# Kernel tuning notes

Hardware: AMD Instinct MI355X
Metric: run time of the kernel (lower is better)

Reference implementation:

```python
import jax, jax.numpy as jnp
import numpy as np
import math

B, L, OBS, ACT = 2, 1024, 64, 16
OE, AE, RE, TE = 512, 256, 128, 128
C, H, NL, FF = 1024, 16, 4, 4096
DH = C // H


def setup_inputs():
    key = jax.random.key(0)
    ks = jax.random.split(key, 20)
    def nrm(k, shape, std=1.0):
        return jax.random.normal(k, shape, jnp.float32) * std
    kb = jax.random.split(ks[19], 12)
    return {
        'obs_seq': nrm(ks[0], (B, L, OBS)),
        'act_seq': nrm(ks[1], (B, L, ACT)),
        'rew_seq': nrm(ks[2], (B, L, 1)),
        'obs_W': nrm(ks[3], (OBS, OE), OBS ** -0.5), 'obs_b': jnp.zeros((OE,)),
        'act_W': nrm(ks[4], (ACT, AE), ACT ** -0.5), 'act_b': jnp.zeros((AE,)),
        'rew_W': nrm(ks[5], (1, RE), 1.0), 'rew_b': jnp.zeros((RE,)),
        'tr_W': nrm(ks[6], (OBS, TE), OBS ** -0.5), 'tr_b': jnp.zeros((TE,)),
        'bn_gamma': jnp.ones((OBS,)), 'bn_beta': jnp.zeros((OBS,)),
        'ln1_w': jnp.ones((NL, C)), 'ln1_b': jnp.zeros((NL, C)),
        'qkv_W': nrm(kb[0], (NL, C, 3 * C), C ** -0.5), 'qkv_b': jnp.zeros((NL, 3 * C)),
        'out_W': nrm(kb[1], (NL, C, C), C ** -0.5), 'out_b': jnp.zeros((NL, C)),
        'ln2_w': jnp.ones((NL, C)), 'ln2_b': jnp.zeros((NL, C)),
        'fc_W': nrm(kb[2], (NL, C, FF), C ** -0.5), 'fc_b': jnp.zeros((NL, FF)),
        'pj_W': nrm(kb[3], (NL, FF, C), FF ** -0.5), 'pj_b': jnp.zeros((NL, C)),
    }


def _ln(x, w, b):
    m = x.mean(-1, keepdims=True)
    v = ((x - m) ** 2).mean(-1, keepdims=True)
    return (x - m) * jax.lax.rsqrt(v + 1e-5) * w + b


def _forward(obs_seq, act_seq, rew_seq, obs_W, obs_b, act_W, act_b, rew_W, rew_b,
             tr_W, tr_b, bn_gamma, bn_beta, ln1_w, ln1_b, qkv_W, qkv_b, out_W, out_b,
             ln2_w, ln2_b, fc_W, fc_b, pj_W, pj_b):
    # transition branch: prepend first obs, take deltas; BatchNorm1d in training
    # mode uses biased batch stats over (batch, time) per channel.
    full_obs = jnp.concatenate([obs_seq[:, :1], obs_seq], axis=1)  # (B, L+1, OBS)
    obs2 = full_obs[:, :-1]
    tran = full_obs[:, 1:] - full_obs[:, :-1]  # (B, L, OBS)
    tm = tran.mean((0, 1))
    tv = ((tran - tm) ** 2).mean((0, 1))
    tran = (tran - tm) * jax.lax.rsqrt(tv + 1e-5) * bn_gamma + bn_beta
    # encoder_activation is identity
    enc = jnp.concatenate([
        obs2 @ obs_W + obs_b,
        act_seq @ act_W + act_b,
        rew_seq @ rew_W + rew_b,
        tran @ tr_W + tr_b,
    ], axis=-1)  # (B, L, C)
    mask = jnp.tril(jnp.ones((L, L), dtype=bool))

    def block(x, p):
        l1w, l1b, qW, qb, oW, ob, l2w, l2b, fW, fb, pW, pb = p
        h = _ln(x, l1w, l1b)
        q, k, v = jnp.split(h @ qW + qb, 3, axis=-1)
        q, k, v = (t.reshape(B, L, H, DH).transpose(0, 2, 1, 3) for t in (q, k, v))
        s = jnp.einsum('bhqd,bhkd->bhqk', q, k) / math.sqrt(DH)
        s = jnp.where(mask, s, -jnp.inf)
        a = jax.nn.softmax(s, axis=-1)
        o = jnp.einsum('bhqk,bhkd->bhqd', a, v).transpose(0, 2, 1, 3).reshape(B, L, C)
        x = x + o @ oW + ob  # residual + out_proj
        h2 = _ln(x, l2w, l2b)
        x = x + jax.nn.relu(h2 @ fW + fb) @ pW + pb  # MLP residual
        return x, None

    x, _ = jax.lax.scan(block, enc, (ln1_w, ln1_b, qkv_W, qkv_b, out_W, out_b,
                                     ln2_w, ln2_b, fc_W, fc_b, pj_W, pj_b))
    return jnp.tanh(x)


def reference(obs_seq, act_seq, rew_seq, obs_W, obs_b, act_W, act_b, rew_W, rew_b,
              tr_W, tr_b, bn_gamma, bn_beta, ln1_w, ln1_b, qkv_W, qkv_b, out_W, out_b,
              ln2_w, ln2_b, fc_W, fc_b, pj_W, pj_b):
    return _forward(obs_seq, act_seq, rew_seq, obs_W, obs_b, act_W, act_b, rew_W, rew_b,
                    tr_W, tr_b, bn_gamma, bn_beta, ln1_w, ln1_b, qkv_W, qkv_b, out_W, out_b,
                    ln2_w, ln2_b, fc_W, fc_b, pj_W, pj_b)
```

## Files before the change

### kernel.cpp

```cpp
#include <hip/hip_runtime.h>
#include <hip/hip_bf16.h>
#include <math.h>

constexpr int kB   = 2;
constexpr int kL   = 1024;
constexpr int kOBS = 64;
constexpr int kACT = 16;
constexpr int kC   = 1024;
constexpr int kH   = 16;
constexpr int kDH  = 64;
constexpr int kFF  = 4096;
constexpr int kNL  = 4;
constexpr int kRows = kB * kL;
constexpr int kOE = 512, kAE = 256, kRE = 128, kTE = 128;

typedef _Float16 f16x8 __attribute__((ext_vector_type(8)));
typedef _Float16 f16x4 __attribute__((ext_vector_type(4)));
typedef float    f32x4 __attribute__((ext_vector_type(4)));

__device__ __forceinline__ unsigned short f2h(float x) {
    return __builtin_bit_cast(unsigned short, (_Float16)x);
}
__device__ __forceinline__ float h2f(unsigned short x) {
    return (float)__builtin_bit_cast(_Float16, x);
}
__device__ __forceinline__ void gload_lds16(const void* g, void* l) {
    __builtin_amdgcn_global_load_lds(
        (const __attribute__((address_space(1))) unsigned int*)g,
        (__attribute__((address_space(3))) unsigned int*)l, 16, 0, 0);
}

__global__ __launch_bounds__(256) void tran_stats_kernel(
    const float* __restrict__ obs, float* __restrict__ tm, float* __restrict__ tv)
{
    const int f = blockIdx.x;
    const int tid = threadIdx.x;
    float sum = 0.f, sq = 0.f;
    for (int r = tid; r < kRows; r += 256) {
        const int t = r & (kL - 1);
        float d = 0.f;
        if (t > 0) {
            const float cur  = obs[(size_t)r * kOBS + f];
            const float prev = obs[(size_t)(r - 1) * kOBS + f];
            d = cur - prev;
        }
        sum += d; sq += d * d;
    }
    for (int off = 32; off > 0; off >>= 1) {
        sum += __shfl_down(sum, off);
        sq  += __shfl_down(sq, off);
    }
    __shared__ float sa[4], sb[4];
    if ((tid & 63) == 0) { sa[tid >> 6] = sum; sb[tid >> 6] = sq; }
    __syncthreads();
    if (tid == 0) {
        const float ts = sa[0] + sa[1] + sa[2] + sa[3];
        const float tq = sb[0] + sb[1] + sb[2] + sb[3];
        const float m = ts / (float)kRows;
        tm[f] = m;
        tv[f] = tq / (float)kRows - m * m;
    }
}

__global__ __launch_bounds__(256) void encode_kernel(
    const float* __restrict__ obs, const float* __restrict__ act, const float* __restrict__ rew,
    const float* __restrict__ obs_W, const float* __restrict__ obs_b,
    const float* __restrict__ act_W, const float* __restrict__ act_b,
    const float* __restrict__ rew_W, const float* __restrict__ rew_b,
    const float* __restrict__ tr_W,  const float* __restrict__ tr_b,
    const float* __restrict__ bn_g,  const float* __restrict__ bn_b,
    const float* __restrict__ tm,    const float* __restrict__ tv,
    float* __restrict__ enc)
{
    const int row = blockIdx.x;
    const int t = row & (kL - 1);
    const int tid = threadIdx.x;
    __shared__ float s_obs2[kOBS];
    __shared__ float s_tran[kOBS];
    __shared__ float s_act[kACT];
    __shared__ float s_rew;
    if (tid < kOBS) {
        const float cur  = obs[(size_t)row * kOBS + tid];
        const float prev = (t > 0) ? obs[(size_t)(row - 1) * kOBS + tid] : cur;
        s_obs2[tid] = prev;
        const float tr = cur - prev;
        s_tran[tid] = (tr - tm[tid]) * rsqrtf(tv[tid] + 1e-5f) * bn_g[tid] + bn_b[tid];
    } else if (tid < kOBS + kACT) {
        s_act[tid - kOBS] = act[(size_t)row * kACT + (tid - kOBS)];
    } else if (tid == kOBS + kACT) {
        s_rew = rew[row];
    }
    __syncthreads();
    float* er = enc + (size_t)row * kC;
    #pragma unroll
    for (int s = 0; s < 4; ++s) {
        const int c = tid + s * 256;
        float v;
        if (c < kOE) {
            v = obs_b[c];
            #pragma unroll
            for (int k = 0; k < kOBS; ++k) v += s_obs2[k] * obs_W[k * kOE + c];
        } else if (c < kOE + kAE) {
            const int cc = c - kOE;
            v = act_b[cc];
            #pragma unroll
            for (int k = 0; k < kACT; ++k) v += s_act[k] * act_W[k * kAE + cc];
        } else if (c < kOE + kAE + kRE) {
            const int cc = c - (kOE + kAE);
            v = s_rew * rew_W[cc] + rew_b[cc];
        } else {
            const int cc = c - (kOE + kAE + kRE);
            v = tr_b[cc];
            #pragma unroll
            for (int k = 0; k < kOBS; ++k) v += s_tran[k] * tr_W[k * kTE + cc];
        }
        er[c] = v;
    }
}

__global__ __launch_bounds__(256) void ln_kernel(
    const float* __restrict__ x, const float* __restrict__ w,
    const float* __restrict__ b, unsigned short* __restrict__ out)
{
    const int row = blockIdx.x;
    const int tid = threadIdx.x;
    const float4 xv = *reinterpret_cast<const float4*>(&x[(size_t)row * kC + tid * 4]);
    float s = xv.x + xv.y + xv.z + xv.w;
    float q = xv.x * xv.x + xv.y * xv.y + xv.z * xv.z + xv.w * xv.w;
    for (int off = 32; off > 0; off >>= 1) {
        s += __shfl_down(s, off);
        q += __shfl_down(q, off);
    }
    __shared__ float sa[4], sb[4];
    if ((tid & 63) == 0) { sa[tid >> 6] = s; sb[tid >> 6] = q; }
    __syncthreads();
    const float ts = sa[0] + sa[1] + sa[2] + sa[3];
    const float tq = sb[0] + sb[1] + sb[2] + sb[3];
    const float mean = ts * (1.f / kC);
    const float var  = tq * (1.f / kC) - mean * mean;
    const float rstd = rsqrtf(var + 1e-5f);
    const float4 wv = *reinterpret_cast<const float4*>(&w[tid * 4]);
    const float4 bv = *reinterpret_cast<const float4*>(&b[tid * 4]);
    ushort4 o;
    o.x = f2h((xv.x - mean) * rstd * wv.x + bv.x);
    o.y = f2h((xv.y - mean) * rstd * wv.y + bv.y);
    o.z = f2h((xv.z - mean) * rstd * wv.z + bv.z);
    o.w = f2h((xv.w - mean) * rstd * wv.w + bv.w);
    *reinterpret_cast<ushort4*>(&out[(size_t)row * kC + tid * 4]) = o;
}

__global__ __launch_bounds__(256) void reduce_ln_kernel(
    const unsigned short* __restrict__ part,
    const float* __restrict__ w, const float* __restrict__ b,
    float* __restrict__ x, unsigned short* __restrict__ h)
{
    const int row = blockIdx.x;
    const int tid = threadIdx.x;
    const size_t base = (size_t)row * kC + tid * 4;
    float4 xv = *reinterpret_cast<const float4*>(&x[base]);
    #pragma unroll
    for (int z = 0; z < 4; ++z) {
        const ushort4 p = *reinterpret_cast<const ushort4*>(
            &part[(size_t)z * kRows * kC + base]);
        xv.x += h2f(p.x); xv.y += h2f(p.y); xv.z += h2f(p.z); xv.w += h2f(p.w);
    }
    *reinterpret_cast<float4*>(&x[base]) = xv;

    float s = xv.x + xv.y + xv.z + xv.w;
    float q = xv.x * xv.x + xv.y * xv.y + xv.z * xv.z + xv.w * xv.w;
    for (int off = 32; off > 0; off >>= 1) {
        s += __shfl_down(s, off);
        q += __shfl_down(q, off);
    }
    __shared__ float sa[4], sb[4];
    if ((tid & 63) == 0) { sa[tid >> 6] = s; sb[tid >> 6] = q; }
    __syncthreads();
    const float ts = sa[0] + sa[1] + sa[2] + sa[3];
    const float tq = sb[0] + sb[1] + sb[2] + sb[3];
    const float mean = ts * (1.f / kC);
    const float var  = tq * (1.f / kC) - mean * mean;
    const float rstd = rsqrtf(var + 1e-5f);
    const float4 wv = *reinterpret_cast<const float4*>(&w[tid * 4]);
    const float4 bv = *reinterpret_cast<const float4*>(&b[tid * 4]);
    ushort4 o;
    o.x = f2h((xv.x - mean) * rstd * wv.x + bv.x);
    o.y = f2h((xv.y - mean) * rstd * wv.y + bv.y);
    o.z = f2h((xv.z - mean) * rstd * wv.z + bv.z);
    o.w = f2h((xv.w - mean) * rstd * wv.w + bv.w);
    *reinterpret_cast<ushort4*>(&h[base]) = o;
}

__global__ __launch_bounds__(256) void reduce_tanh_kernel(
    const unsigned short* __restrict__ part, float* __restrict__ x)
{
    const size_t base = ((size_t)blockIdx.x * 256 + threadIdx.x) * 4;
    float4 xv = *reinterpret_cast<const float4*>(&x[base]);
    #pragma unroll
    for (int z = 0; z < 4; ++z) {
        const ushort4 p = *reinterpret_cast<const ushort4*>(
            &part[(size_t)z * kRows * kC + base]);
        xv.x += h2f(p.x); xv.y += h2f(p.y); xv.z += h2f(p.z); xv.w += h2f(p.w);
    }
    xv.x = tanhf(xv.x); xv.y = tanhf(xv.y); xv.z = tanhf(xv.z); xv.w = tanhf(xv.w);
    *reinterpret_cast<float4*>(&x[base]) = xv;
}

__device__ __forceinline__ void convT_tile(
    const float* __restrict__ W, unsigned short* __restrict__ WT,
    int K, int N, int k0, int n0, int tid)
{
    __shared__ unsigned short t[64][68];
    const int r = tid >> 4, c4 = (tid & 15) * 4;
    #pragma unroll
    for (int s = 0; s < 4; ++s) {
        const int rr = r + s * 16;
        const float4 v = *reinterpret_cast<const float4*>(&W[(size_t)(k0 + rr) * N + n0 + c4]);
        t[rr][c4 + 0] = f2h(v.x);
        t[rr][c4 + 1] = f2h(v.y);
        t[rr][c4 + 2] = f2h(v.z);
        t[rr][c4 + 3] = f2h(v.w);
    }
    __syncthreads();
    #pragma unroll
    for (int s = 0; s < 4; ++s) {
        const int rn = r + s * 16;
        ushort4 o;
        o.x = t[c4 + 0][rn];
        o.y = t[c4 + 1][rn];
        o.z = t[c4 + 2][rn];
        o.w = t[c4 + 3][rn];
        *reinterpret_cast<ushort4*>(&WT[(size_t)(n0 + rn) * K + k0 + c4]) = o;
    }
}

__global__ __launch_bounds__(256) void convert_layer_kernel(
    const float* __restrict__ qW, const float* __restrict__ oW,
    const float* __restrict__ fW, const float* __restrict__ pW,
    unsigned short* __restrict__ qWT, unsigned short* __restrict__ oWT,
    unsigned short* __restrict__ fWT, unsigned short* __restrict__ pWT)
{
    int bid = blockIdx.x;
    const int tid = threadIdx.x;
    if (bid < 768)  {
        convT_tile(qW, qWT, 1024, 3072, (bid / 48) * 64, (bid % 48) * 64, tid);
    } else if (bid < 1024) {
        bid -= 768;
        convT_tile(oW, oWT, 1024, 1024, (bid / 16) * 64, (bid % 16) * 64, tid);
    } else if (bid < 2048) {
        bid -= 1024;
        convT_tile(fW, fWT, 1024, 4096, (bid / 64) * 64, (bid % 64) * 64, tid);
    } else {
        bid -= 2048;
        convT_tile(pW, pWT, 4096, 1024, (bid / 16) * 64, (bid % 16) * 64, tid);
    }
}

template<int RELU, int RES, int MODE>
__global__ __launch_bounds__(256) void gemm_f16_kernel(
    const unsigned short* __restrict__ A,
    const unsigned short* __restrict__ BT,
    const float* __restrict__ bias,
    float* __restrict__ Cf, unsigned short* __restrict__ Ch,
    unsigned short* __restrict__ Cv,
    int M, int N, int K)
{
    __shared__ __align__(16) unsigned short As[2][128 * 64];
    __shared__ __align__(16) unsigned short Bs[2][128 * 64];
    const int tid = threadIdx.x;
    const int lane = tid & 63;
    const int wv   = tid >> 6;
    const int wr = wv >> 1, wc = wv & 1;

    const int nx  = gridDim.x;
    const int nxy = gridDim.x * gridDim.y;
    int flat = blockIdx.x + nx * blockIdx.y + nxy * blockIdx.z;
    const int cpx = (nxy * gridDim.z) >> 3;
    flat = (flat & 7) * cpx + (flat >> 3);
    const int bx = flat % nx;
    const int by = (flat / nx) % gridDim.y;
    const int bz = flat / nxy;

    const int bm = by * 128;
    const int bn = bx * 128;
    const int ksz  = K / gridDim.z;
    const int kbeg = bz * ksz;
    const int kend = kbeg + ksz;

    const int grow = tid >> 3;
    const int gs   = (tid & 7) ^ (grow & 7);

    const int fr = lane & 15;
    const int kb = lane >> 4;

    auto stage = [&](int k0, int buf) {
        #pragma unroll
        for (int c = 0; c < 4; ++c) {
            gload_lds16(A  + (size_t)(bm + c * 32 + grow) * K + k0 + gs * 8,
                        (char*)&As[buf][0] + c * 4096 + wv * 1024);
            gload_lds16(BT + (size_t)(bn + c * 32 + grow) * K + k0 + gs * 8,
                        (char*)&Bs[buf][0] + c * 4096 + wv * 1024);
        }
    };

    f32x4 acc[4][4] = {};

    stage(kbeg, 0);
    __syncthreads();
    int cur = 0;
    for (int k0 = kbeg; k0 < kend; k0 += 64) {
        f16x8 a[2][4], b[2][4];
        #pragma unroll
        for (int kf = 0; kf < 2; ++kf) {
            #pragma unroll
            for (int m = 0; m < 4; ++m) {
                const int row = wr * 64 + m * 16 + fr;
                a[kf][m] = *reinterpret_cast<const f16x8*>(
                    &As[cur][row * 64 + (((kf * 4 + kb) ^ (row & 7)) * 8)]);
            }
            #pragma unroll
            for (int n = 0; n < 4; ++n) {
                const int row = wc * 64 + n * 16 + fr;
                b[kf][n] = *reinterpret_cast<const f16x8*>(
                    &Bs[cur][row * 64 + (((kf * 4 + kb) ^ (row & 7)) * 8)]);
            }
        }
        if (k0 + 64 < kend) stage(k0 + 64, cur ^ 1);
        #pragma unroll
        for (int kf = 0; kf < 2; ++kf)
            #pragma unroll
            for (int m = 0; m < 4; ++m)
                #pragma unroll
                for (int n = 0; n < 4; ++n)
                    acc[m][n] = __builtin_amdgcn_mfma_f32_16x16x32_f16(
                        a[kf][m], b[kf][n], acc[m][n], 0, 0, 0);

        __syncthreads();
        cur ^= 1;
    }

    const int fq = lane >> 4;
    if (MODE == 5) {
        unsigned short* pp = Ch + (size_t)bz * M * N;
        const bool addb = (bz == 0);
        #pragma unroll
        for (int n = 0; n < 4; ++n) {
            const int c = bn + wc * 64 + n * 16 + fr;
            const float bv = addb ? bias[c] : 0.f;
            #pragma unroll
            for (int m = 0; m < 4; ++m) {
                #pragma unroll
                for (int j = 0; j < 4; ++j) {
                    const int r = bm + wr * 64 + m * 16 + fq * 4 + j;
                    pp[(size_t)r * N + c] = f2h(acc[m][n][j] + bv);
                }
            }
        }
        return;
    }
    if (MODE == 2) {
        if (bn < 2 * kC) {
            #pragma unroll
            for (int n = 0; n < 4; ++n) {
                const int c = bn + wc * 64 + n * 16 + fr;
                const float bv = bias[c];
                #pragma unroll
                for (int m = 0; m < 4; ++m) {
                    #pragma unroll
                    for (int j = 0; j < 4; ++j) {
                        const int r = bm + wr * 64 + m * 16 + fq * 4 + j;
                        Ch[(size_t)r * (2 * kC) + c] = f2h(acc[m][n][j] + bv);
                    }
                }
            }
        } else {
            #pragma unroll
            for (int n = 0; n < 4; ++n) {
                const int c  = bn + wc * 64 + n * 16 + fr;
                const int cc = c - 2 * kC;
                const int hh = cc >> 6, dd = cc & 63;
                const float bv = bias[c];
                #pragma unroll
                for (int m = 0; m < 4; ++m) {
                    const int rr = bm + wr * 64 + m * 16 + fq * 4;
                    const int bb = rr >> 10, t0 = rr & 1023;
                    f16x4 pk;
                    #pragma unroll
                    for (int j = 0; j < 4; ++j) pk[j] = (_Float16)(acc[m][n][j] + bv);
                    *reinterpret_cast<f16x4*>(
                        &Cv[((size_t)(bb * kH + hh) * kDH + dd) * kL + t0]) = pk;
                }
            }
        }
        return;
    }
    #pragma unroll
    for (int n = 0; n < 4; ++n) {
        const int c = bn + wc * 64 + n * 16 + fr;
        const float bv = bias[c];
        #pragma unroll
        for (int m = 0; m < 4; ++m) {
            #pragma unroll
            for (int j = 0; j < 4; ++j) {
                const int r = bm + wr * 64 + m * 16 + fq * 4 + j;
                float v = acc[m][n][j] + bv;
                if (RES)  v += Cf[(size_t)r * N + c];
                if (RELU) v = fmaxf(v, 0.f);
                if (MODE == 1) Ch[(size_t)r * N + c] = f2h(v);
                else           Cf[(size_t)r * N + c] = v;
            }
        }
    }
}

__device__ __forceinline__ int swz(int row, int slot) {
    return row * 64 + ((slot ^ (row & 7)) * 8);
}

__global__ __launch_bounds__(256) void attn_mfma_kernel(
    const unsigned short* __restrict__ qk,
    const unsigned short* __restrict__ vt,
    unsigned short* __restrict__ o)
{
    const int bid = blockIdx.x;
    const int bh  = bid & 31;
    const int qb  = ((bid >> 5) + bh) & 15;
    const int b   = bh >> 4;
    const int h   = bh & 15;
    const int tid  = threadIdx.x;
    const int lane = tid & 63;
    const int wv   = tid >> 6;
    const int fr = lane & 15;
    const int g  = lane >> 4;

    __shared__ __align__(16) unsigned short Ks[64 * 64];
    __shared__ __align__(16) unsigned short Vts[64 * 64];
    __shared__ __align__(16) unsigned short Ps[64 * 64];

    const int qlo = qb * 64;
    const int qg_row = qlo + wv * 16 + fr;

    f16x8 qfrag[2];
    {
        const unsigned short* qg = &qk[(size_t)(b * kL + qg_row) * (2 * kC) + h * kDH];
        #pragma unroll
        for (int kf = 0; kf < 2; ++kf) {
            f16x8 v = *reinterpret_cast<const f16x8*>(&qg[(kf * 4 + g) * 8]);
            #pragma unroll
            for (int i = 0; i < 8; ++i) v[i] *= (_Float16)0.125f;
            qfrag[kf] = v;
        }
    }

    const int sr = tid >> 2;
    const int ss = tid & 3;
    const unsigned short* kbase = &qk[(size_t)(b * kL) * (2 * kC) + kC + h * kDH];
    const unsigned short* vbase = &vt[(size_t)(b * kH + h) * kDH * kL];

    f16x8 kc0 = *reinterpret_cast<const f16x8*>(&kbase[(size_t)sr * (2 * kC) + ss * 8]);
    f16x8 kc1 = *reinterpret_cast<const f16x8*>(&kbase[(size_t)sr * (2 * kC) + (ss + 4) * 8]);
    f16x8 vc0 = *reinterpret_cast<const f16x8*>(&vbase[(size_t)sr * kL + ss * 8]);
    f16x8 vc1 = *reinterpret_cast<const f16x8*>(&vbase[(size_t)sr * kL + (ss + 4) * 8]);

    float m = -INFINITY, l = 0.f;
    f32x4 acc_o[4] = {};

    for (int k0 = 0; k0 <= qlo; k0 += 64) {
        asm volatile("s_waitcnt lgkmcnt(0)" ::: "memory");
        __builtin_amdgcn_sched_barrier(0);
        __builtin_amdgcn_s_barrier();
        __builtin_amdgcn_sched_barrier(0);

        *reinterpret_cast<f16x8*>(&Ks[swz(sr, ss)])      = kc0;
        *reinterpret_cast<f16x8*>(&Ks[swz(sr, ss + 4)])  = kc1;
        *reinterpret_cast<f16x8*>(&Vts[swz(sr, ss)])     = vc0;
        *reinterpret_cast<f16x8*>(&Vts[swz(sr, ss + 4)]) = vc1;

        if (k0 + 64 <= qlo) {
            kc0 = *reinterpret_cast<const f16x8*>(&kbase[(size_t)(k0 + 64 + sr) * (2 * kC) + ss * 8]);
            kc1 = *reinterpret_cast<const f16x8*>(&kbase[(size_t)(k0 + 64 + sr) * (2 * kC) + (ss + 4) * 8]);
            vc0 = *reinterpret_cast<const f16x8*>(&vbase[(size_t)sr * kL + k0 + 64 + ss * 8]);
            vc1 = *reinterpret_cast<const f16x8*>(&vbase[(size_t)sr * kL + k0 + 64 + (ss + 4) * 8]);
        }

        asm volatile("s_waitcnt lgkmcnt(0)" ::: "memory");
        __builtin_amdgcn_sched_barrier(0);
        __builtin_amdgcn_s_barrier();
        __builtin_amdgcn_sched_barrier(0);

        f32x4 acc_s[4] = {};
        #pragma unroll
        for (int kf = 0; kf < 2; ++kf) {
            #pragma unroll
            for (int n = 0; n < 4; ++n) {
                const f16x8 kfr = *reinterpret_cast<const f16x8*>(&Ks[swz(n * 16 + fr, kf * 4 + g)]);
                acc_s[n] = __builtin_amdgcn_mfma_f32_16x16x32_f16(kfr, qfrag[kf], acc_s[n], 0, 0, 0);
            }
        }

        if (k0 == qlo) {
            #pragma unroll
            for (int n = 0; n < 4; ++n)
                #pragma unroll
                for (int j = 0; j < 4; ++j)
                    if (k0 + n * 16 + g * 4 + j > qg_row) acc_s[n][j] = -INFINITY;
        }

        float mx = -INFINITY;
        #pragma unroll
        for (int n = 0; n < 4; ++n)
            #pragma unroll
            for (int j = 0; j < 4; ++j) mx = fmaxf(mx, acc_s[n][j]);
        mx = fmaxf(mx, __shfl_xor(mx, 16));
        mx = fmaxf(mx, __shfl_xor(mx, 32));
        const float mn  = fmaxf(m, mx);
        const float fac = __expf(m - mn);
        float p[4][4];
        float psum = 0.f;
        #pragma unroll
        for (int n = 0; n < 4; ++n)
            #pragma unroll
            for (int j = 0; j < 4; ++j) { p[n][j] = __expf(acc_s[n][j] - mn); psum += p[n][j]; }
        psum += __shfl_xor(psum, 16);
        psum += __shfl_xor(psum, 32);
        l = l * fac + psum;
        m = mn;
        #pragma unroll
        for (int dt = 0; dt < 4; ++dt)
            #pragma unroll
            for (int j = 0; j < 4; ++j) acc_o[dt][j] *= fac;

        #pragma unroll
        for (int n = 0; n < 4; ++n) {
            f16x4 pk;
            #pragma unroll
            for (int j = 0; j < 4; ++j) pk[j] = (_Float16)p[n][j];
            *reinterpret_cast<f16x4*>(&Ps[swz(wv * 16 + fr, 2 * n + (g >> 1)) + (g & 1) * 4]) = pk;
        }

        #pragma unroll
        for (int kf = 0; kf < 2; ++kf) {
            const f16x8 pf = *reinterpret_cast<const f16x8*>(&Ps[swz(wv * 16 + fr, kf * 4 + g)]);
            #pragma unroll
            for (int dt = 0; dt < 4; ++dt) {
                const f16x8 vf = *reinterpret_cast<const f16x8*>(&Vts[swz(dt * 16 + fr, kf * 4 + g)]);
                acc_o[dt] = __builtin_amdgcn_mfma_f32_16x16x32_f16(vf, pf, acc_o[dt], 0, 0, 0);
            }
        }
    }

    const float rl = 1.f / l;
    unsigned short* ob = &o[(size_t)(b * kL + qg_row) * kC + h * kDH];
    #pragma unroll
    for (int dt = 0; dt < 4; ++dt) {
        f16x4 pk;
        #pragma unroll
        for (int j = 0; j < 4; ++j) pk[j] = (_Float16)(acc_o[dt][j] * rl);
        *reinterpret_cast<f16x4*>(&ob[dt * 16 + g * 4]) = pk;
    }
}

extern "C" void kernel_launch(void* const* d_in, const int* in_sizes, int n_in,
                              void* d_out, int out_size, void* d_ws, size_t ws_size,
                              hipStream_t stream)
{
    (void)in_sizes; (void)n_in; (void)out_size; (void)ws_size;
    const float* obs    = (const float*)d_in[0];
    const float* act    = (const float*)d_in[1];
    const float* rew    = (const float*)d_in[2];
    const float* obs_W  = (const float*)d_in[3];
    const float* obs_b  = (const float*)d_in[4];
    const float* act_W  = (const float*)d_in[5];
    const float* act_b  = (const float*)d_in[6];
    const float* rew_W  = (const float*)d_in[7];
    const float* rew_b  = (const float*)d_in[8];
    const float* tr_W   = (const float*)d_in[9];
    const float* tr_b   = (const float*)d_in[10];
    const float* bn_g   = (const float*)d_in[11];
    const float* bn_b   = (const float*)d_in[12];
    const float* ln1_w  = (const float*)d_in[13];
    const float* ln1_b  = (const float*)d_in[14];
    const float* qkv_W  = (const float*)d_in[15];
    const float* qkv_b  = (const float*)d_in[16];
    const float* out_W  = (const float*)d_in[17];
    const float* out_b  = (const float*)d_in[18];
    const float* ln2_w  = (const float*)d_in[19];
    const float* ln2_b  = (const float*)d_in[20];
    const float* fc_W   = (const float*)d_in[21];
    const float* fc_b   = (const float*)d_in[22];
    const float* pj_W   = (const float*)d_in[23];
    const float* pj_b   = (const float*)d_in[24];

    float* x  = (float*)d_out;
    float* ws = (float*)d_ws;
    float* tm   = ws;
    float* tv   = ws + 64;
    unsigned short* wbuf  = (unsigned short*)(ws + 128);
    unsigned short* h_hf  = wbuf + 12582912;
    unsigned short* ao_hf = h_hf + (size_t)kRows * kC;
    unsigned short* ff_hf = ao_hf + (size_t)kRows * kC;
    unsigned short* qk_hf = ff_hf + (size_t)kRows * kFF;
    unsigned short* vt_hf = qk_hf + (size_t)kRows * 2 * kC;
    unsigned short* part  = qk_hf;
    unsigned short* qWT = wbuf;
    unsigned short* oWT = qWT + 3 * kC * kC;
    unsigned short* fWT = oWT + kC * kC;
    unsigned short* pWT = fWT + kC * kFF;

    tran_stats_kernel<<<kOBS, 256, 0, stream>>>(obs, tm, tv);
    encode_kernel<<<kRows, 256, 0, stream>>>(obs, act, rew,
        obs_W, obs_b, act_W, act_b, rew_W, rew_b, tr_W, tr_b, bn_g, bn_b, tm, tv, x);
    ln_kernel<<<kRows, 256, 0, stream>>>(x, ln1_w, ln1_b, h_hf);

    for (int lyr = 0; lyr < kNL; ++lyr) {
        const float* qW = qkv_W + (size_t)lyr * kC * 3 * kC;
        const float* qB = qkv_b + (size_t)lyr * 3 * kC;
        const float* oW = out_W + (size_t)lyr * kC * kC;
        const float* oB = out_b + (size_t)lyr * kC;
        const float* fW = fc_W + (size_t)lyr * kC * kFF;
        const float* fB = fc_b + (size_t)lyr * kFF;
        const float* pW = pj_W + (size_t)lyr * kFF * kC;
        const float* pB = pj_b + (size_t)lyr * kC;

        convert_layer_kernel<<<3072, 256, 0, stream>>>(
            qW, oW, fW, pW, qWT, oWT, fWT, pWT);

        gemm_f16_kernel<0,0,2><<<dim3(3 * kC / 128, kRows / 128), 256, 0, stream>>>(
            h_hf, qWT, qB, nullptr, qk_hf, vt_hf, kRows, 3 * kC, kC);
        attn_mfma_kernel<<<dim3(512), 256, 0, stream>>>(qk_hf, vt_hf, ao_hf);
        gemm_f16_kernel<0,0,5><<<dim3(kC / 128, kRows / 128, 4), 256, 0, stream>>>(
            ao_hf, oWT, oB, nullptr, part, nullptr, kRows, kC, kC);
        reduce_ln_kernel<<<kRows, 256, 0, stream>>>(
            part, ln2_w + lyr * kC, ln2_b + lyr * kC, x, h_hf);
        gemm_f16_kernel<1,0,1><<<dim3(kFF / 128, kRows / 128), 256, 0, stream>>>(
            h_hf, fWT, fB, nullptr, ff_hf, nullptr, kRows, kFF, kC);
        gemm_f16_kernel<0,0,5><<<dim3(kC / 128, kRows / 128, 4), 256, 0, stream>>>(
            ff_hf, pWT, pB, nullptr, part, nullptr, kRows, kC, kFF);
        if (lyr < kNL - 1) {
            reduce_ln_kernel<<<kRows, 256, 0, stream>>>(
                part, ln1_w + (lyr + 1) * kC, ln1_b + (lyr + 1) * kC, x, h_hf);
        } else {
            reduce_tanh_kernel<<<kRows * kC / 1024, 256, 0, stream>>>(part, x);
        }
    }
}
```

Before: 553.8 us.

## Fuse encoder with first LayerNorm; lazy softmax rescale and MFMA priority in attention

Merges the encoder and the first LayerNorm into one kernel, so the per-row statistics come from registers instead of a second launch that rereads the encoder output. In the attention kernel, the online-softmax rescale of the accumulator is skipped while the new row max exceeds the running max by at most a threshold. The MFMA sections are also wrapped in s_setprio hints. The lazy rescale lets exponentials reach values up to e^8, which is safe in fp32 but relies on fp16 P values staying in range.

```diff
diff --git a/kernel.cpp b/kernel.cpp
--- a/kernel.cpp
+++ b/kernel.cpp
@@ -62,7 +62,7 @@
     }
 }
 
-__global__ __launch_bounds__(256) void encode_kernel(
+__global__ __launch_bounds__(256) void encode_ln_kernel(
     const float* __restrict__ obs, const float* __restrict__ act, const float* __restrict__ rew,
     const float* __restrict__ obs_W, const float* __restrict__ obs_b,
     const float* __restrict__ act_W, const float* __restrict__ act_b,
@@ -70,7 +70,8 @@
     const float* __restrict__ tr_W,  const float* __restrict__ tr_b,
     const float* __restrict__ bn_g,  const float* __restrict__ bn_b,
     const float* __restrict__ tm,    const float* __restrict__ tv,
-    float* __restrict__ enc)
+    const float* __restrict__ ln_w,  const float* __restrict__ ln_b,
+    float* __restrict__ enc, unsigned short* __restrict__ h)
 {
     const int row = blockIdx.x;
     const int t = row & (kL - 1);
@@ -92,6 +93,7 @@
     }
     __syncthreads();
     float* er = enc + (size_t)row * kC;
+    float vals[4];
     #pragma unroll
     for (int s = 0; s < 4; ++s) {
         const int c = tid + s * 256;
@@ -115,18 +117,10 @@
             for (int k = 0; k < kOBS; ++k) v += s_tran[k] * tr_W[k * kTE + cc];
         }
         er[c] = v;
-    }
-}
-
-__global__ __launch_bounds__(256) void ln_kernel(
-    const float* __restrict__ x, const float* __restrict__ w,
-    const float* __restrict__ b, unsigned short* __restrict__ out)
-{
-    const int row = blockIdx.x;
-    const int tid = threadIdx.x;
-    const float4 xv = *reinterpret_cast<const float4*>(&x[(size_t)row * kC + tid * 4]);
-    float s = xv.x + xv.y + xv.z + xv.w;
-    float q = xv.x * xv.x + xv.y * xv.y + xv.z * xv.z + xv.w * xv.w;
+        vals[s] = v;
+    }
+    float s = vals[0] + vals[1] + vals[2] + vals[3];
+    float q = vals[0]*vals[0] + vals[1]*vals[1] + vals[2]*vals[2] + vals[3]*vals[3];
     for (int off = 32; off > 0; off >>= 1) {
         s += __shfl_down(s, off);
         q += __shfl_down(q, off);
@@ -139,14 +133,12 @@
     const float mean = ts * (1.f / kC);
     const float var  = tq * (1.f / kC) - mean * mean;
     const float rstd = rsqrtf(var + 1e-5f);
-    const float4 wv = *reinterpret_cast<const float4*>(&w[tid * 4]);
-    const float4 bv = *reinterpret_cast<const float4*>(&b[tid * 4]);
-    ushort4 o;
-    o.x = f2h((xv.x - mean) * rstd * wv.x + bv.x);
-    o.y = f2h((xv.y - mean) * rstd * wv.y + bv.y);
-    o.z = f2h((xv.z - mean) * rstd * wv.z + bv.z);
-    o.w = f2h((xv.w - mean) * rstd * wv.w + bv.w);
-    *reinterpret_cast<ushort4*>(&out[(size_t)row * kC + tid * 4]) = o;
+    unsigned short* hr = h + (size_t)row * kC;
+    #pragma unroll
+    for (int sx = 0; sx < 4; ++sx) {
+        const int c = tid + sx * 256;
+        hr[c] = f2h((vals[sx] - mean) * rstd * ln_w[c] + ln_b[c]);
+    }
 }
 
 __global__ __launch_bounds__(256) void reduce_ln_kernel(
@@ -488,6 +480,7 @@
         __builtin_amdgcn_sched_barrier(0);
 
         f32x4 acc_s[4] = {};
+        __builtin_amdgcn_s_setprio(1);
         #pragma unroll
         for (int kf = 0; kf < 2; ++kf) {
             #pragma unroll
@@ -496,6 +489,7 @@
                 acc_s[n] = __builtin_amdgcn_mfma_f32_16x16x32_f16(kfr, qfrag[kf], acc_s[n], 0, 0, 0);
             }
         }
+        __builtin_amdgcn_s_setprio(0);
 
         if (k0 == qlo) {
             #pragma unroll
@@ -512,22 +506,33 @@
             for (int j = 0; j < 4; ++j) mx = fmaxf(mx, acc_s[n][j]);
         mx = fmaxf(mx, __shfl_xor(mx, 16));
         mx = fmaxf(mx, __shfl_xor(mx, 32));
-        const float mn  = fmaxf(m, mx);
-        const float fac = __expf(m - mn);
+
         float p[4][4];
         float psum = 0.f;
-        #pragma unroll
-        for (int n = 0; n < 4; ++n)
-            #pragma unroll
-            for (int j = 0; j < 4; ++j) { p[n][j] = __expf(acc_s[n][j] - mn); psum += p[n][j]; }
-        psum += __shfl_xor(psum, 16);
-        psum += __shfl_xor(psum, 32);
-        l = l * fac + psum;
-        m = mn;
-        #pragma unroll
-        for (int dt = 0; dt < 4; ++dt)
-            #pragma unroll
-            for (int j = 0; j < 4; ++j) acc_o[dt][j] *= fac;
+        if (__all(mx - m <= 8.f)) {
+            #pragma unroll
+            for (int n = 0; n < 4; ++n)
+                #pragma unroll
+                for (int j = 0; j < 4; ++j) { p[n][j] = __expf(acc_s[n][j] - m); psum += p[n][j]; }
+            psum += __shfl_xor(psum, 16);
+            psum += __shfl_xor(psum, 32);
+            l += psum;
+        } else {
+            const float mn  = fmaxf(m, mx);
+            const float fac = __expf(m - mn);
+            #pragma unroll
+            for (int n = 0; n < 4; ++n)
+                #pragma unroll
+                for (int j = 0; j < 4; ++j) { p[n][j] = __expf(acc_s[n][j] - mn); psum += p[n][j]; }
+            psum += __shfl_xor(psum, 16);
+            psum += __shfl_xor(psum, 32);
+            l = l * fac + psum;
+            m = mn;
+            #pragma unroll
+            for (int dt = 0; dt < 4; ++dt)
+                #pragma unroll
+                for (int j = 0; j < 4; ++j) acc_o[dt][j] *= fac;
+        }
 
         #pragma unroll
         for (int n = 0; n < 4; ++n) {
@@ -537,6 +542,7 @@
             *reinterpret_cast<f16x4*>(&Ps[swz(wv * 16 + fr, 2 * n + (g >> 1)) + (g & 1) * 4]) = pk;
         }
 
+        __builtin_amdgcn_s_setprio(1);
         #pragma unroll
         for (int kf = 0; kf < 2; ++kf) {
             const f16x8 pf = *reinterpret_cast<const f16x8*>(&Ps[swz(wv * 16 + fr, kf * 4 + g)]);
@@ -546,6 +552,7 @@
                 acc_o[dt] = __builtin_amdgcn_mfma_f32_16x16x32_f16(vf, pf, acc_o[dt], 0, 0, 0);
             }
         }
+        __builtin_amdgcn_s_setprio(0);
     }
 
     const float rl = 1.f / l;
@@ -607,9 +614,9 @@
     unsigned short* pWT = fWT + kC * kFF;
 
     tran_stats_kernel<<<kOBS, 256, 0, stream>>>(obs, tm, tv);
-    encode_kernel<<<kRows, 256, 0, stream>>>(obs, act, rew,
-        obs_W, obs_b, act_W, act_b, rew_W, rew_b, tr_W, tr_b, bn_g, bn_b, tm, tv, x);
-    ln_kernel<<<kRows, 256, 0, stream>>>(x, ln1_w, ln1_b, h_hf);
+    encode_ln_kernel<<<kRows, 256, 0, stream>>>(obs, act, rew,
+        obs_W, obs_b, act_W, act_b, rew_W, rew_b, tr_W, tr_b, bn_g, bn_b, tm, tv,
+        ln1_w, ln1_b, x, h_hf);
 
     for (int lyr = 0; lyr < kNL; ++lyr) {
         const float* qW = qkv_W + (size_t)lyr * kC * 3 * kC;
```

After: 555.0 us, median of 2. No clear change (+0.2%).
